# Kernel optimization log

Hardware: AMD Instinct MI355X
Metric: run time of the kernel (lower is better)

Reference implementation:

```python
import jax, jax.numpy as jnp
import numpy as np

DIM, HEADS, WIN = 256, 8, 8
HD = DIM // HEADS
SCALE = HD ** -0.5


def _rel_index(w):
    # Swin-style relative position index, computed statically in numpy
    coords = np.stack(np.meshgrid(np.arange(w), np.arange(w), indexing='ij'))  # (2,w,w)
    cf = coords.reshape(2, -1)                      # (2, w*w)
    rel = (cf[:, :, None] - cf[:, None, :]).transpose(1, 2, 0)  # (w*w, w*w, 2)
    rel = rel.copy()
    rel[:, :, 0] += w - 1
    rel[:, :, 1] += w - 1
    rel[:, :, 0] *= 2 * w - 1
    return rel.sum(-1)                              # (w*w, w*w)

REL_IDX = _rel_index(WIN)


def setup_inputs() -> dict:
    key = jax.random.key(0)
    ks = jax.random.split(key, 6)
    B, C, D, H, W = 8, DIM, 100, WIN, WIN
    return {
        'x': jax.random.normal(ks[0], (B, C, D, H, W), jnp.float32),
        'dwconv_w': jax.random.normal(ks[1], (C, C, 1, 3, 3), jnp.float32) * 0.02,
        'dwconv_b': jnp.zeros((C,), jnp.float32),
        'qkv_w': jax.random.normal(ks[2], (3 * C, C), jnp.float32) * 0.02,
        'qkv_b': jnp.zeros((3 * C,), jnp.float32),
        'proj_w': jax.random.normal(ks[3], (C, C), jnp.float32) * 0.02,
        'proj_b': jnp.zeros((C,), jnp.float32),
        'rpb_table': jax.random.normal(ks[4], ((2 * WIN - 1) ** 2, HEADS), jnp.float32) * 0.02,
    }


def reference(x, dwconv_w, dwconv_b, qkv_w, qkv_b, proj_w, proj_b, rpb_table):
    B, C, D, H, W = x.shape
    N = H * W
    # 'dwconv': full Conv3d, kernel (1,3,3), padding (0,1,1)
    xl = jax.lax.conv_general_dilated(
        x, dwconv_w, window_strides=(1, 1, 1),
        padding=[(0, 0), (1, 1), (1, 1)],
        dimension_numbers=('NCDHW', 'OIDHW', 'NCDHW'),
    ) + dwconv_b[None, :, None, None, None]
    # qkv: 1x1x1 conv == pointwise linear over channels
    qkv = jnp.einsum('oc,bcdhw->bodhw', qkv_w, xl) + qkv_b[None, :, None, None, None]
    # channel dim layout: (three, head, head_dim)
    qkv = qkv.reshape(B, 3, HEADS, HD, D, N)
    q, k, v = qkv[:, 0], qkv[:, 1], qkv[:, 2]      # each (B, HEADS, HD, D, N)
    attn = jnp.einsum('bhcdn,bhcdm->bdhnm', q * SCALE, k)  # (B, D, HEADS, N, N)
    bias = rpb_table[REL_IDX.reshape(-1)].reshape(N, N, HEADS).transpose(2, 0, 1)
    attn = jax.nn.softmax(attn + bias[None, None], axis=-1)
    xa = jnp.einsum('bdhnm,bhcdm->bhcdn', attn, v)  # (B, HEADS, HD, D, N)
    xa = xa.reshape(B, C, D, H, W)                  # channel = (head, head_dim)
    out = jnp.einsum('oc,bcdhw->bodhw', proj_w, xa) + proj_b[None, :, None, None, None]
    return out
```

## Files before the change

kernel.cpp:

```cpp
#include <hip/hip_runtime.h>
#include <cstdint>
#include <cstddef>

#define SCALEQ 0.17677669529663689f

typedef _Float16 half_t;
typedef _Float16 half8   __attribute__((ext_vector_type(8)));
typedef _Float16 half4v  __attribute__((ext_vector_type(4)));
typedef float    float4v __attribute__((ext_vector_type(4)));

#define GLDS16(gp, lp)                                                        \
  __builtin_amdgcn_global_load_lds(                                           \
      (const __attribute__((address_space(1))) void*)(gp),                    \
      (__attribute__((address_space(3))) void*)(lp), 16, 0, 0)

#define WAIT_LDS()                                                            \
  do {                                                                        \
    asm volatile("s_waitcnt lgkmcnt(0)" ::: "memory");                        \
    __builtin_amdgcn_sched_barrier(0);                                        \
  } while (0)

__global__ __launch_bounds__(256) void prep_all(
    const float* __restrict__ x, const float* __restrict__ dwconv_w,
    const float* __restrict__ qkv_w, const float* __restrict__ proj_w,
    const float* __restrict__ rpb, half_t* __restrict__ xq,
    half_t* __restrict__ Wt, half_t* __restrict__ qw16,
    half_t* __restrict__ pw16, float* __restrict__ btab) {
  __shared__ float tile[128 * 65];
  const int blk = blockIdx.x, t = threadIdx.x;
  if (blk < 800) {
    const int bd = blk, b = bd / 100, d = bd % 100;
    for (int hf = 0; hf < 2; ++hf) {
      for (int i = 0; i < 32; ++i) {
        int idx = i * 256 + t, c = idx >> 6, hw = idx & 63;
        tile[c * 65 + hw] = x[(size_t)((b * 256 + hf * 128 + c) * 100 + d) * 64 + hw];
      }
      __syncthreads();
#pragma unroll
      for (int i = 0; i < 4; ++i) {
        int chunk = i * 256 + t;
        int hw = chunk >> 4, c8 = chunk & 15;
        half8 h;
#pragma unroll
        for (int j = 0; j < 8; ++j) h[j] = (half_t)tile[(c8 * 8 + j) * 65 + hw];
        *(half8*)(xq + (size_t)(bd * 64 + hw) * 256 + hf * 128 + c8 * 8) = h;
      }
      __syncthreads();
    }
  } else if (blk < 944) {
    const int base = (blk - 800) * 4096;
#pragma unroll
    for (int i = 0; i < 16; ++i) {
      int idx = base + i * 256 + t;
      int tap = idx >> 16;
      int og = (idx >> 12) & 15, kh = (idx >> 9) & 7;
      int l15o = (idx >> 5) & 15, c5 = idx & 31;
      int o = og * 16 + l15o, c = kh * 32 + c5;
      Wt[idx] = (half_t)dwconv_w[(o * 256 + c) * 9 + tap];
    }
  } else if (blk < 1040) {
    const int base = (blk - 944) * 2048;
#pragma unroll
    for (int i = 0; i < 8; ++i) {
      int idx = base + i * 256 + t;
      float v = qkv_w[idx];
      if (idx < 65536) v *= SCALEQ;
      qw16[idx] = (half_t)v;
    }
  } else if (blk < 1072) {
    const int base = (blk - 1040) * 2048;
#pragma unroll
    for (int i = 0; i < 8; ++i) {
      int idx = base + i * 256 + t;
      pw16[idx] = (half_t)proj_w[idx];
    }
  } else {
    const int base = (blk - 1072) * 2048;
#pragma unroll
    for (int i = 0; i < 8; ++i) {
      int idx = base + i * 256 + t;
      int hd = idx >> 12, n = (idx >> 6) & 63, m = idx & 63;
      int h1 = n >> 3, w1 = n & 7, h2 = m >> 3, w2 = m & 7;
      int ridx = (h1 - h2 + 7) * 15 + (w1 - w2 + 7);
      btab[idx] = rpb[ridx * 8 + hd];
    }
  }
}

__global__ __launch_bounds__(512)
__attribute__((amdgpu_waves_per_eu(4, 4))) void fused_all(
    const half_t* __restrict__ xqg, const half_t* __restrict__ Wt,
    const float* __restrict__ convb, const half_t* __restrict__ qw,
    const float* __restrict__ qkvb, const float* __restrict__ btab,
    const half_t* __restrict__ pw, const float* __restrict__ projb,
    float* __restrict__ out32) {
  __shared__ __align__(16) half_t LS[36864];
  const int bd = blockIdx.x;
  const int tid = threadIdx.x;
  const int wave = tid >> 6, lane = tid & 63;
  const int l15 = lane & 15, quad = lane >> 4;
  const int head = wave;

  half_t* xlp = LS;
  half_t* xa = LS;
  float* T = (float*)LS;
  half_t* xpl = LS + 16384;
  half_t* buf = LS + 16384 + wave * 2560;

  const half_t* Wq0 = qw + head * 32 * 256;
  const half_t* Wk0 = qw + 65536 + head * 32 * 256;
  const half_t* Wv0 = qw + 131072 + head * 32 * 256;

  {
    const char* src = (const char*)(xqg + (size_t)bd * 16384);
    const int cid = wave * 64 + lane;
#pragma unroll
    for (int i = 0; i < 4; ++i) {
      const int chunkid = i * 512 + cid;
      const int row = chunkid >> 5, p = chunkid & 31;
      const int g = (p & 24) | ((p ^ row) & 7);
      GLDS16(src + row * 512 + g * 16, (char*)xpl + (i * 512 + wave * 64) * 16);
    }
    if (tid < 32) {
      half8 z = {};
      *(half8*)(xpl + 64 * 256 + tid * 8) = z;
    }
  }
  __syncthreads();

  {
    const int wwl = l15 & 7, hb = l15 >> 3;
    float4v acc[2][4];
#pragma unroll
    for (int mi = 0; mi < 2; ++mi)
#pragma unroll
      for (int ni = 0; ni < 4; ++ni) {
        float4v z = {0.f, 0.f, 0.f, 0.f};
        acc[mi][ni] = z;
      }
    const half_t* wv0 = Wt + (wave * 2) * 4096 + l15 * 32 + quad * 8;
#pragma unroll 1
    for (int tap = 0; tap < 9; ++tap) {
      const int th = tap / 3, tw = tap - th * 3;
      const half_t* wt = wv0 + tap * 65536;
      const int ww = wwl + tw;
      const int okw = (ww >= 1) & (ww <= 8);
      int rowv[4];
#pragma unroll
      for (int ni = 0; ni < 4; ++ni) {
        const int hh = hb + th + ni * 2;
        const int ok = okw & (hh >= 1) & (hh <= 8);
        rowv[ni] = ok ? ((hh - 1) * 8 + (ww - 1)) : 64;
      }
#pragma unroll
      for (int kh = 0; kh < 8; ++kh) {
        half8 af0 = *(const half8*)(wt + kh * 512);
        half8 af1 = *(const half8*)(wt + 4096 + kh * 512);
        half8 bf[4];
#pragma unroll
        for (int ni = 0; ni < 4; ++ni) {
          const int r = rowv[ni];
          bf[ni] = *(const half8*)&xpl[r * 256 + (((kh * 4 + quad) ^ (r & 7)) * 8)];
        }
#pragma unroll
        for (int ni = 0; ni < 4; ++ni) {
          acc[0][ni] = __builtin_amdgcn_mfma_f32_16x16x32_f16(af0, bf[ni], acc[0][ni], 0, 0, 0);
          acc[1][ni] = __builtin_amdgcn_mfma_f32_16x16x32_f16(af1, bf[ni], acc[1][ni], 0, 0, 0);
        }
      }
    }
#pragma unroll
    for (int mi = 0; mi < 2; ++mi) {
      const int o4 = wave * 32 + mi * 16 + quad * 4;
      const float4v b4 = *(const float4v*)&convb[o4];
      const int chunk = o4 >> 3;
      const int sub = (quad & 1) * 4;
#pragma unroll
      for (int ni = 0; ni < 4; ++ni) {
        const int px = ni * 16 + l15;
        half4v h;
        h.x = (half_t)(acc[mi][ni].x + b4.x);
        h.y = (half_t)(acc[mi][ni].y + b4.y);
        h.z = (half_t)(acc[mi][ni].z + b4.z);
        h.w = (half_t)(acc[mi][ni].w + b4.w);
        *(half4v*)&xlp[px * 256 + ((chunk ^ (px & 7)) * 8) + sub] = h;
      }
    }
  }

  __syncthreads();

  half8 aq[4];
  {
    float4v acc[2][4];
#pragma unroll
    for (int mi = 0; mi < 2; ++mi)
#pragma unroll
      for (int ni = 0; ni < 4; ++ni) {
        float4v z = {0.f, 0.f, 0.f, 0.f};
        acc[mi][ni] = z;
      }
#pragma unroll
    for (int kh = 0; kh < 8; ++kh) {
      half8 w0 = *(const half8*)(Wq0 + l15 * 256 + kh * 32 + quad * 8);
      half8 w1 = *(const half8*)(Wq0 + (16 + l15) * 256 + kh * 32 + quad * 8);
      half8 bf[4];
#pragma unroll
      for (int ni = 0; ni < 4; ++ni) {
        int r = ni * 16 + l15;
        bf[ni] = *(const half8*)&xlp[r * 256 + (((kh * 4 + quad) ^ (r & 7)) * 8)];
      }
#pragma unroll
      for (int ni = 0; ni < 4; ++ni) {
        acc[0][ni] = __builtin_amdgcn_mfma_f32_16x16x32_f16(w0, bf[ni], acc[0][ni], 0, 0, 0);
        acc[1][ni] = __builtin_amdgcn_mfma_f32_16x16x32_f16(w1, bf[ni], acc[1][ni], 0, 0, 0);
      }
    }
#pragma unroll
    for (int mi = 0; mi < 2; ++mi) {
      const float4v b4 = *(const float4v*)&qkvb[head * 32 + mi * 16 + quad * 4];
#pragma unroll
      for (int ni = 0; ni < 4; ++ni) {
        half4v h;
        h.x = (half_t)(acc[mi][ni].x + b4.x * SCALEQ);
        h.y = (half_t)(acc[mi][ni].y + b4.y * SCALEQ);
        h.z = (half_t)(acc[mi][ni].z + b4.z * SCALEQ);
        h.w = (half_t)(acc[mi][ni].w + b4.w * SCALEQ);
        *(half4v*)(buf + (ni * 16 + l15) * 40 + mi * 16 + quad * 4) = h;
      }
    }
    WAIT_LDS();
#pragma unroll
    for (int i = 0; i < 4; ++i)
      aq[i] = *(const half8*)(buf + (i * 16 + l15) * 40 + quad * 8);
    WAIT_LDS();
  }

  half8 bk[4];
  {
    float4v acc[2][4];
#pragma unroll
    for (int mi = 0; mi < 2; ++mi)
#pragma unroll
      for (int ni = 0; ni < 4; ++ni) {
        float4v z = {0.f, 0.f, 0.f, 0.f};
        acc[mi][ni] = z;
      }
#pragma unroll
    for (int kh = 0; kh < 8; ++kh) {
      half8 w0 = *(const half8*)(Wk0 + l15 * 256 + kh * 32 + quad * 8);
      half8 w1 = *(const half8*)(Wk0 + (16 + l15) * 256 + kh * 32 + quad * 8);
      half8 bf[4];
#pragma unroll
      for (int ni = 0; ni < 4; ++ni) {
        int r = ni * 16 + l15;
        bf[ni] = *(const half8*)&xlp[r * 256 + (((kh * 4 + quad) ^ (r & 7)) * 8)];
      }
#pragma unroll
      for (int ni = 0; ni < 4; ++ni) {
        acc[0][ni] = __builtin_amdgcn_mfma_f32_16x16x32_f16(w0, bf[ni], acc[0][ni], 0, 0, 0);
        acc[1][ni] = __builtin_amdgcn_mfma_f32_16x16x32_f16(w1, bf[ni], acc[1][ni], 0, 0, 0);
      }
    }
#pragma unroll
    for (int mi = 0; mi < 2; ++mi) {
      const float4v b4 = *(const float4v*)&qkvb[256 + head * 32 + mi * 16 + quad * 4];
#pragma unroll
      for (int ni = 0; ni < 4; ++ni) {
        half4v h;
        h.x = (half_t)(acc[mi][ni].x + b4.x);
        h.y = (half_t)(acc[mi][ni].y + b4.y);
        h.z = (half_t)(acc[mi][ni].z + b4.z);
        h.w = (half_t)(acc[mi][ni].w + b4.w);
        *(half4v*)(buf + (ni * 16 + l15) * 40 + mi * 16 + quad * 4) = h;
      }
    }
    WAIT_LDS();
#pragma unroll
    for (int i = 0; i < 4; ++i)
      bk[i] = *(const half8*)(buf + (i * 16 + l15) * 40 + quad * 8);
    WAIT_LDS();
  }

  {
    float4v acc[2][4];
#pragma unroll
    for (int mi = 0; mi < 2; ++mi)
#pragma unroll
      for (int ni = 0; ni < 4; ++ni) {
        float4v z = {0.f, 0.f, 0.f, 0.f};
        acc[mi][ni] = z;
      }
#pragma unroll
    for (int kh = 0; kh < 8; ++kh) {
      half8 w0 = *(const half8*)(Wv0 + l15 * 256 + kh * 32 + quad * 8);
      half8 w1 = *(const half8*)(Wv0 + (16 + l15) * 256 + kh * 32 + quad * 8);
      half8 bf[4];
#pragma unroll
      for (int ni = 0; ni < 4; ++ni) {
        int r = ni * 16 + l15;
        bf[ni] = *(const half8*)&xlp[r * 256 + (((kh * 4 + quad) ^ (r & 7)) * 8)];
      }
#pragma unroll
      for (int ni = 0; ni < 4; ++ni) {
        acc[0][ni] = __builtin_amdgcn_mfma_f32_16x16x32_f16(w0, bf[ni], acc[0][ni], 0, 0, 0);
        acc[1][ni] = __builtin_amdgcn_mfma_f32_16x16x32_f16(w1, bf[ni], acc[1][ni], 0, 0, 0);
      }
    }
#pragma unroll
    for (int mi = 0; mi < 2; ++mi) {
      const float4v b4 = *(const float4v*)&qkvb[512 + head * 32 + mi * 16 + quad * 4];
#pragma unroll
      for (int ni = 0; ni < 4; ++ni) {
#pragma unroll
        for (int iv = 0; iv < 4; ++iv)
          buf[(mi * 16 + quad * 4 + iv) * 72 + ni * 16 + l15] =
              (half_t)(acc[mi][ni][iv] + b4[iv]);
      }
    }
  }

  const float* bh = btab + head * 4096;
  float4v s[4][4];
#pragma unroll
  for (int ni = 0; ni < 4; ++ni)
#pragma unroll
    for (int mi = 0; mi < 4; ++mi) {
      float4v z = {0.f, 0.f, 0.f, 0.f};
      s[ni][mi] = __builtin_amdgcn_mfma_f32_16x16x32_f16(aq[ni], bk[mi], z, 0, 0, 0);
    }
#pragma unroll
  for (int ni = 0; ni < 4; ++ni)
#pragma unroll
    for (int i = 0; i < 4; ++i) {
      const int n = ni * 16 + quad * 4 + i;
#pragma unroll
      for (int mi = 0; mi < 4; ++mi)
        s[ni][mi][i] += bh[n * 64 + mi * 16 + l15];
    }
  float inv[4][4];
#pragma unroll
  for (int ni = 0; ni < 4; ++ni)
#pragma unroll
    for (int i = 0; i < 4; ++i) {
      float mx = fmaxf(fmaxf(s[ni][0][i], s[ni][1][i]), fmaxf(s[ni][2][i], s[ni][3][i]));
      for (int off = 1; off < 16; off <<= 1) mx = fmaxf(mx, __shfl_xor(mx, off));
      float sum = 0.f;
#pragma unroll
      for (int mi = 0; mi < 4; ++mi) {
        float e = __expf(s[ni][mi][i] - mx);
        s[ni][mi][i] = e;
        sum += e;
      }
      for (int off = 1; off < 16; off <<= 1) sum += __shfl_xor(sum, off);
      inv[ni][i] = 1.0f / sum;
    }
  half4v ph[4][4];
#pragma unroll
  for (int ni = 0; ni < 4; ++ni)
#pragma unroll
    for (int mi = 0; mi < 4; ++mi)
#pragma unroll
      for (int i = 0; i < 4; ++i)
        ph[ni][mi][i] = (half_t)(s[ni][mi][i] * inv[ni][i]);

  WAIT_LDS();
  half8 av[2][2];
#pragma unroll
  for (int ci = 0; ci < 2; ++ci)
#pragma unroll
    for (int k2 = 0; k2 < 2; ++k2)
      av[ci][k2] = *(const half8*)(buf + (ci * 16 + l15) * 72 + k2 * 32 + quad * 8);
  WAIT_LDS();

  float4v oa[2][4];
#pragma unroll
  for (int ci = 0; ci < 2; ++ci)
#pragma unroll
    for (int ni = 0; ni < 4; ++ni) {
      float4v z = {0.f, 0.f, 0.f, 0.f};
      oa[ci][ni] = z;
    }
#pragma unroll
  for (int k2 = 0; k2 < 2; ++k2) {
#pragma unroll
    for (int mi2 = 0; mi2 < 2; ++mi2) {
      const int mi = k2 * 2 + mi2;
#pragma unroll
      for (int ni = 0; ni < 4; ++ni)
#pragma unroll
        for (int i = 0; i < 4; ++i) {
          const int n = ni * 16 + quad * 4 + i;
          buf[n * 40 + mi2 * 16 + l15] = ph[ni][mi][i];
        }
    }
    WAIT_LDS();
    half8 bp[4];
#pragma unroll
    for (int ni = 0; ni < 4; ++ni)
      bp[ni] = *(const half8*)(buf + (ni * 16 + l15) * 40 + quad * 8);
    WAIT_LDS();
#pragma unroll
    for (int ni = 0; ni < 4; ++ni)
#pragma unroll
      for (int ci = 0; ci < 2; ++ci)
        oa[ci][ni] = __builtin_amdgcn_mfma_f32_16x16x32_f16(av[ci][k2], bp[ni], oa[ci][ni], 0, 0, 0);
  }

  __syncthreads();

#pragma unroll
  for (int ci = 0; ci < 2; ++ci)
#pragma unroll
    for (int ni = 0; ni < 4; ++ni) {
      half4v h = {(half_t)oa[ci][ni].x, (half_t)oa[ci][ni].y,
                  (half_t)oa[ci][ni].z, (half_t)oa[ci][ni].w};
      *(half4v*)(xa + (ni * 16 + l15) * 264 + head * 32 + ci * 16 + quad * 4) = h;
    }
  __syncthreads();

  const half_t* Wp0 = pw + wave * 32 * 256;
  float4v pacc[2][4];
#pragma unroll
  for (int mi = 0; mi < 2; ++mi)
#pragma unroll
    for (int ni = 0; ni < 4; ++ni) {
      float4v z = {0.f, 0.f, 0.f, 0.f};
      pacc[mi][ni] = z;
    }
#pragma unroll
  for (int kh = 0; kh < 8; ++kh) {
    half8 w0 = *(const half8*)(Wp0 + l15 * 256 + kh * 32 + quad * 8);
    half8 w1 = *(const half8*)(Wp0 + (16 + l15) * 256 + kh * 32 + quad * 8);
    half8 bf[4];
#pragma unroll
    for (int ni = 0; ni < 4; ++ni)
      bf[ni] = *(const half8*)&xa[(ni * 16 + l15) * 264 + kh * 32 + quad * 8];
#pragma unroll
    for (int ni = 0; ni < 4; ++ni) {
      pacc[0][ni] = __builtin_amdgcn_mfma_f32_16x16x32_f16(w0, bf[ni], pacc[0][ni], 0, 0, 0);
      pacc[1][ni] = __builtin_amdgcn_mfma_f32_16x16x32_f16(w1, bf[ni], pacc[1][ni], 0, 0, 0);
    }
  }
#pragma unroll
  for (int mi = 0; mi < 2; ++mi) {
    const float4v b4 = *(const float4v*)&projb[wave * 32 + mi * 16 + quad * 4];
#pragma unroll
    for (int ni = 0; ni < 4; ++ni) {
      pacc[mi][ni].x += b4.x;
      pacc[mi][ni].y += b4.y;
      pacc[mi][ni].z += b4.z;
      pacc[mi][ni].w += b4.w;
    }
  }

  const int b = bd / 100, d = bd % 100;
  const size_t bdbase = (size_t)b * 1638400 + (size_t)d * 64;
  const int tr = tid >> 3;
  const int col0 = (tid & 7) * 4;
  for (int r = 0; r < 4; ++r) {
    __syncthreads();
    if ((wave >> 1) == r) {
      const int rb = (wave & 1) * 32;
#pragma unroll
      for (int mi = 0; mi < 2; ++mi)
#pragma unroll
        for (int ni = 0; ni < 4; ++ni)
#pragma unroll
          for (int iv = 0; iv < 4; ++iv)
            T[(rb + mi * 16 + quad * 4 + iv) * 68 + ni * 16 + l15] = pacc[mi][ni][iv];
    }
    __syncthreads();
    const int o = r * 64 + tr;
    float* dst = out32 + bdbase + (size_t)o * 6400 + col0;
    const float* srcT = &T[tr * 68 + col0];
    float4v v0 = *(const float4v*)srcT;
    float4v v1 = *(const float4v*)(srcT + 32);
    __builtin_nontemporal_store(v0, (float4v*)dst);
    __builtin_nontemporal_store(v1, (float4v*)(dst + 32));
  }
}

extern "C" void kernel_launch(void* const* d_in, const int* in_sizes, int n_in,
                              void* d_out, int out_size, void* d_ws, size_t ws_size,
                              hipStream_t stream) {
  const float* x        = (const float*)d_in[0];
  const float* dwconv_w = (const float*)d_in[1];
  const float* dwconv_b = (const float*)d_in[2];
  const float* qkv_w    = (const float*)d_in[3];
  const float* qkv_b    = (const float*)d_in[4];
  const float* proj_w   = (const float*)d_in[5];
  const float* proj_b   = (const float*)d_in[6];
  const float* rpb      = (const float*)d_in[7];
  float* out = (float*)d_out;

  char* ws = (char*)d_ws;
  size_t off = 0;
  half_t* xq   = (half_t*)(ws + off); off += 26214400;
  half_t* Wt   = (half_t*)(ws + off); off += 1179648;
  half_t* qw16 = (half_t*)(ws + off); off += 393216;
  half_t* pw16 = (half_t*)(ws + off); off += 131072;
  float*  btab = (float*)(ws + off);  off += 131072;

  prep_all<<<1088, 256, 0, stream>>>(x, dwconv_w, qkv_w, proj_w, rpb,
                                     xq, Wt, qw16, pw16, btab);
  fused_all<<<800, 512, 0, stream>>>(xq, Wt, dwconv_b, qw16, qkv_b, btab,
                                     pw16, proj_b, out);
}
```

Before: 269.7 us.

## Shrink LDS footprint to raise occupancy by reading conv input from global

The conv stage now reads its input tile straight from global memory, with a padded zero row added to the prep-stage layout, instead of staging it in LDS. The per-wave LDS scratch is halved by transposing Q, K, V and P in two halves, and occupancy is raised from 4 to 6 waves per EU. This trades LDS traffic and its bank-swizzled reads for uncached-in-LDS global/L2 reads during the conv, and the larger wave count may push up register pressure.

```diff
diff --git a/kernel.cpp b/kernel.cpp
--- a/kernel.cpp
+++ b/kernel.cpp
@@ -8,11 +8,6 @@
 typedef _Float16 half8   __attribute__((ext_vector_type(8)));
 typedef _Float16 half4v  __attribute__((ext_vector_type(4)));
 typedef float    float4v __attribute__((ext_vector_type(4)));
-
-#define GLDS16(gp, lp)                                                        \
-  __builtin_amdgcn_global_load_lds(                                           \
-      (const __attribute__((address_space(1))) void*)(gp),                    \
-      (__attribute__((address_space(3))) void*)(lp), 16, 0, 0)
 
 #define WAIT_LDS()                                                            \
   do {                                                                        \
@@ -30,6 +25,10 @@
   const int blk = blockIdx.x, t = threadIdx.x;
   if (blk < 800) {
     const int bd = blk, b = bd / 100, d = bd % 100;
+    if (t < 32) {
+      half8 z = {};
+      *(half8*)(xq + ((size_t)bd * 65 + 64) * 256 + t * 8) = z;
+    }
     for (int hf = 0; hf < 2; ++hf) {
       for (int i = 0; i < 32; ++i) {
         int idx = i * 256 + t, c = idx >> 6, hw = idx & 63;
@@ -43,7 +42,7 @@
         half8 h;
 #pragma unroll
         for (int j = 0; j < 8; ++j) h[j] = (half_t)tile[(c8 * 8 + j) * 65 + hw];
-        *(half8*)(xq + (size_t)(bd * 64 + hw) * 256 + hf * 128 + c8 * 8) = h;
+        *(half8*)(xq + ((size_t)bd * 65 + hw) * 256 + hf * 128 + c8 * 8) = h;
       }
       __syncthreads();
     }
@@ -88,13 +87,13 @@
 }
 
 __global__ __launch_bounds__(512)
-__attribute__((amdgpu_waves_per_eu(4, 4))) void fused_all(
+__attribute__((amdgpu_waves_per_eu(6, 6))) void fused_all(
     const half_t* __restrict__ xqg, const half_t* __restrict__ Wt,
     const float* __restrict__ convb, const half_t* __restrict__ qw,
     const float* __restrict__ qkvb, const float* __restrict__ btab,
     const half_t* __restrict__ pw, const float* __restrict__ projb,
     float* __restrict__ out32) {
-  __shared__ __align__(16) half_t LS[36864];
+  __shared__ __align__(16) half_t LS[26624];
   const int bd = blockIdx.x;
   const int tid = threadIdx.x;
   const int wave = tid >> 6, lane = tid & 63;
@@ -104,29 +103,12 @@
   half_t* xlp = LS;
   half_t* xa = LS;
   float* T = (float*)LS;
-  half_t* xpl = LS + 16384;
-  half_t* buf = LS + 16384 + wave * 2560;
+  half_t* buf = LS + 16384 + wave * 1280;
 
   const half_t* Wq0 = qw + head * 32 * 256;
   const half_t* Wk0 = qw + 65536 + head * 32 * 256;
   const half_t* Wv0 = qw + 131072 + head * 32 * 256;
-
-  {
-    const char* src = (const char*)(xqg + (size_t)bd * 16384);
-    const int cid = wave * 64 + lane;
-#pragma unroll
-    for (int i = 0; i < 4; ++i) {
-      const int chunkid = i * 512 + cid;
-      const int row = chunkid >> 5, p = chunkid & 31;
-      const int g = (p & 24) | ((p ^ row) & 7);
-      GLDS16(src + row * 512 + g * 16, (char*)xpl + (i * 512 + wave * 64) * 16);
-    }
-    if (tid < 32) {
-      half8 z = {};
-      *(half8*)(xpl + 64 * 256 + tid * 8) = z;
-    }
-  }
-  __syncthreads();
+  const half_t* xb = xqg + (size_t)bd * 16640;
 
   {
     const int wwl = l15 & 7, hb = l15 >> 3;
@@ -158,10 +140,8 @@
         half8 af1 = *(const half8*)(wt + 4096 + kh * 512);
         half8 bf[4];
 #pragma unroll
-        for (int ni = 0; ni < 4; ++ni) {
-          const int r = rowv[ni];
-          bf[ni] = *(const half8*)&xpl[r * 256 + (((kh * 4 + quad) ^ (r & 7)) * 8)];
-        }
+        for (int ni = 0; ni < 4; ++ni)
+          bf[ni] = *(const half8*)(xb + rowv[ni] * 256 + kh * 32 + quad * 8);
 #pragma unroll
         for (int ni = 0; ni < 4; ++ni) {
           acc[0][ni] = __builtin_amdgcn_mfma_f32_16x16x32_f16(af0, bf[ni], acc[0][ni], 0, 0, 0);
@@ -217,23 +197,27 @@
       }
     }
 #pragma unroll
-    for (int mi = 0; mi < 2; ++mi) {
-      const float4v b4 = *(const float4v*)&qkvb[head * 32 + mi * 16 + quad * 4];
-#pragma unroll
-      for (int ni = 0; ni < 4; ++ni) {
-        half4v h;
-        h.x = (half_t)(acc[mi][ni].x + b4.x * SCALEQ);
-        h.y = (half_t)(acc[mi][ni].y + b4.y * SCALEQ);
-        h.z = (half_t)(acc[mi][ni].z + b4.z * SCALEQ);
-        h.w = (half_t)(acc[mi][ni].w + b4.w * SCALEQ);
-        *(half4v*)(buf + (ni * 16 + l15) * 40 + mi * 16 + quad * 4) = h;
-      }
-    }
-    WAIT_LDS();
-#pragma unroll
-    for (int i = 0; i < 4; ++i)
-      aq[i] = *(const half8*)(buf + (i * 16 + l15) * 40 + quad * 8);
-    WAIT_LDS();
+    for (int h2 = 0; h2 < 2; ++h2) {
+#pragma unroll
+      for (int mi = 0; mi < 2; ++mi) {
+        const float4v b4 = *(const float4v*)&qkvb[head * 32 + mi * 16 + quad * 4];
+#pragma unroll
+        for (int nj = 0; nj < 2; ++nj) {
+          const int ni = h2 * 2 + nj;
+          half4v h;
+          h.x = (half_t)(acc[mi][ni].x + b4.x * SCALEQ);
+          h.y = (half_t)(acc[mi][ni].y + b4.y * SCALEQ);
+          h.z = (half_t)(acc[mi][ni].z + b4.z * SCALEQ);
+          h.w = (half_t)(acc[mi][ni].w + b4.w * SCALEQ);
+          *(half4v*)(buf + (nj * 16 + l15) * 40 + mi * 16 + quad * 4) = h;
+        }
+      }
+      WAIT_LDS();
+#pragma unroll
+      for (int j = 0; j < 2; ++j)
+        aq[h2 * 2 + j] = *(const half8*)(buf + (j * 16 + l15) * 40 + quad * 8);
+      WAIT_LDS();
+    }
   }
 
   half8 bk[4];
@@ -263,25 +247,30 @@
       }
     }
 #pragma unroll
-    for (int mi = 0; mi < 2; ++mi) {
-      const float4v b4 = *(const float4v*)&qkvb[256 + head * 32 + mi * 16 + quad * 4];
-#pragma unroll
-      for (int ni = 0; ni < 4; ++ni) {
-        half4v h;
-        h.x = (half_t)(acc[mi][ni].x + b4.x);
-        h.y = (half_t)(acc[mi][ni].y + b4.y);
-        h.z = (half_t)(acc[mi][ni].z + b4.z);
-        h.w = (half_t)(acc[mi][ni].w + b4.w);
-        *(half4v*)(buf + (ni * 16 + l15) * 40 + mi * 16 + quad * 4) = h;
-      }
-    }
-    WAIT_LDS();
-#pragma unroll
-    for (int i = 0; i < 4; ++i)
-      bk[i] = *(const half8*)(buf + (i * 16 + l15) * 40 + quad * 8);
-    WAIT_LDS();
-  }
-
+    for (int h2 = 0; h2 < 2; ++h2) {
+#pragma unroll
+      for (int mi = 0; mi < 2; ++mi) {
+        const float4v b4 = *(const float4v*)&qkvb[256 + head * 32 + mi * 16 + quad * 4];
+#pragma unroll
+        for (int nj = 0; nj < 2; ++nj) {
+          const int ni = h2 * 2 + nj;
+          half4v h;
+          h.x = (half_t)(acc[mi][ni].x + b4.x);
+          h.y = (half_t)(acc[mi][ni].y + b4.y);
+          h.z = (half_t)(acc[mi][ni].z + b4.z);
+          h.w = (half_t)(acc[mi][ni].w + b4.w);
+          *(half4v*)(buf + (nj * 16 + l15) * 40 + mi * 16 + quad * 4) = h;
+        }
+      }
+      WAIT_LDS();
+#pragma unroll
+      for (int j = 0; j < 2; ++j)
+        bk[h2 * 2 + j] = *(const half8*)(buf + (j * 16 + l15) * 40 + quad * 8);
+      WAIT_LDS();
+    }
+  }
+
+  half8 av[2][2];
   {
     float4v acc[2][4];
 #pragma unroll
@@ -311,12 +300,16 @@
     for (int mi = 0; mi < 2; ++mi) {
       const float4v b4 = *(const float4v*)&qkvb[512 + head * 32 + mi * 16 + quad * 4];
 #pragma unroll
-      for (int ni = 0; ni < 4; ++ni) {
+      for (int ni = 0; ni < 4; ++ni)
 #pragma unroll
         for (int iv = 0; iv < 4; ++iv)
-          buf[(mi * 16 + quad * 4 + iv) * 72 + ni * 16 + l15] =
+          buf[(quad * 4 + iv) * 72 + ni * 16 + l15] =
               (half_t)(acc[mi][ni][iv] + b4[iv]);
-      }
+      WAIT_LDS();
+#pragma unroll
+      for (int k2 = 0; k2 < 2; ++k2)
+        av[mi][k2] = *(const half8*)(buf + l15 * 72 + k2 * 32 + quad * 8);
+      WAIT_LDS();
     }
   }
 
@@ -364,15 +357,6 @@
       for (int i = 0; i < 4; ++i)
         ph[ni][mi][i] = (half_t)(s[ni][mi][i] * inv[ni][i]);
 
-  WAIT_LDS();
-  half8 av[2][2];
-#pragma unroll
-  for (int ci = 0; ci < 2; ++ci)
-#pragma unroll
-    for (int k2 = 0; k2 < 2; ++k2)
-      av[ci][k2] = *(const half8*)(buf + (ci * 16 + l15) * 72 + k2 * 32 + quad * 8);
-  WAIT_LDS();
-
   float4v oa[2][4];
 #pragma unroll
   for (int ci = 0; ci < 2; ++ci)
@@ -384,27 +368,31 @@
 #pragma unroll
   for (int k2 = 0; k2 < 2; ++k2) {
 #pragma unroll
-    for (int mi2 = 0; mi2 < 2; ++mi2) {
-      const int mi = k2 * 2 + mi2;
-#pragma unroll
-      for (int ni = 0; ni < 4; ++ni)
-#pragma unroll
-        for (int i = 0; i < 4; ++i) {
-          const int n = ni * 16 + quad * 4 + i;
-          buf[n * 40 + mi2 * 16 + l15] = ph[ni][mi][i];
+    for (int rh = 0; rh < 2; ++rh) {
+#pragma unroll
+      for (int nj = 0; nj < 2; ++nj) {
+        const int ni = rh * 2 + nj;
+#pragma unroll
+        for (int mi2 = 0; mi2 < 2; ++mi2) {
+          const int mi = k2 * 2 + mi2;
+#pragma unroll
+          for (int i = 0; i < 4; ++i)
+            buf[(nj * 16 + quad * 4 + i) * 36 + mi2 * 16 + l15] = ph[ni][mi][i];
         }
-    }
-    WAIT_LDS();
-    half8 bp[4];
-#pragma unroll
-    for (int ni = 0; ni < 4; ++ni)
-      bp[ni] = *(const half8*)(buf + (ni * 16 + l15) * 40 + quad * 8);
-    WAIT_LDS();
-#pragma unroll
-    for (int ni = 0; ni < 4; ++ni)
-#pragma unroll
-      for (int ci = 0; ci < 2; ++ci)
-        oa[ci][ni] = __builtin_amdgcn_mfma_f32_16x16x32_f16(av[ci][k2], bp[ni], oa[ci][ni], 0, 0, 0);
+      }
+      WAIT_LDS();
+      half8 bpn[2];
+#pragma unroll
+      for (int nj = 0; nj < 2; ++nj)
+        bpn[nj] = *(const half8*)(buf + (nj * 16 + l15) * 36 + quad * 8);
+      WAIT_LDS();
+#pragma unroll
+      for (int nj = 0; nj < 2; ++nj)
+#pragma unroll
+        for (int ci = 0; ci < 2; ++ci)
+          oa[ci][rh * 2 + nj] = __builtin_amdgcn_mfma_f32_16x16x32_f16(
+              av[ci][k2], bpn[nj], oa[ci][rh * 2 + nj], 0, 0, 0);
+    }
   }
 
   __syncthreads();
@@ -496,7 +484,7 @@
 
   char* ws = (char*)d_ws;
   size_t off = 0;
-  half_t* xq   = (half_t*)(ws + off); off += 26214400;
+  half_t* xq   = (half_t*)(ws + off); off += 26624000;
   half_t* Wt   = (half_t*)(ws + off); off += 1179648;
   half_t* qw16 = (half_t*)(ws + off); off += 393216;
   half_t* pw16 = (half_t*)(ws + off); off += 131072;
```

Result: slower. 561.5 us (+108.2%).

## Fuse input transpose and fp16 cast into main fused kernel

Applied to the files above, without the earlier changes.

Removes the per-(b,d) transpose/convert stage from the prep kernel and has the fused kernel read fp32 x directly, transpose it through LDS, convert it to half and write the swizzled layout. This drops a 26 MB intermediate write and its read-back, and shrinks the prep grid. In exchange the main kernel does extra LDS round trips, two more barriers and strided global reads before the conv stage can start.

```diff
diff --git a/kernel.cpp b/kernel.cpp
--- a/kernel.cpp
+++ b/kernel.cpp
@@ -8,11 +8,6 @@
 typedef _Float16 half8   __attribute__((ext_vector_type(8)));
 typedef _Float16 half4v  __attribute__((ext_vector_type(4)));
 typedef float    float4v __attribute__((ext_vector_type(4)));
-
-#define GLDS16(gp, lp)                                                        \
-  __builtin_amdgcn_global_load_lds(                                           \
-      (const __attribute__((address_space(1))) void*)(gp),                    \
-      (__attribute__((address_space(3))) void*)(lp), 16, 0, 0)
 
 #define WAIT_LDS()                                                            \
   do {                                                                        \
@@ -20,35 +15,14 @@
     __builtin_amdgcn_sched_barrier(0);                                        \
   } while (0)
 
-__global__ __launch_bounds__(256) void prep_all(
-    const float* __restrict__ x, const float* __restrict__ dwconv_w,
-    const float* __restrict__ qkv_w, const float* __restrict__ proj_w,
-    const float* __restrict__ rpb, half_t* __restrict__ xq,
+__global__ __launch_bounds__(256) void prep_w(
+    const float* __restrict__ dwconv_w, const float* __restrict__ qkv_w,
+    const float* __restrict__ proj_w, const float* __restrict__ rpb,
     half_t* __restrict__ Wt, half_t* __restrict__ qw16,
     half_t* __restrict__ pw16, float* __restrict__ btab) {
-  __shared__ float tile[128 * 65];
   const int blk = blockIdx.x, t = threadIdx.x;
-  if (blk < 800) {
-    const int bd = blk, b = bd / 100, d = bd % 100;
-    for (int hf = 0; hf < 2; ++hf) {
-      for (int i = 0; i < 32; ++i) {
-        int idx = i * 256 + t, c = idx >> 6, hw = idx & 63;
-        tile[c * 65 + hw] = x[(size_t)((b * 256 + hf * 128 + c) * 100 + d) * 64 + hw];
-      }
-      __syncthreads();
-#pragma unroll
-      for (int i = 0; i < 4; ++i) {
-        int chunk = i * 256 + t;
-        int hw = chunk >> 4, c8 = chunk & 15;
-        half8 h;
-#pragma unroll
-        for (int j = 0; j < 8; ++j) h[j] = (half_t)tile[(c8 * 8 + j) * 65 + hw];
-        *(half8*)(xq + (size_t)(bd * 64 + hw) * 256 + hf * 128 + c8 * 8) = h;
-      }
-      __syncthreads();
-    }
-  } else if (blk < 944) {
-    const int base = (blk - 800) * 4096;
+  if (blk < 144) {
+    const int base = blk * 4096;
 #pragma unroll
     for (int i = 0; i < 16; ++i) {
       int idx = base + i * 256 + t;
@@ -58,8 +32,8 @@
       int o = og * 16 + l15o, c = kh * 32 + c5;
       Wt[idx] = (half_t)dwconv_w[(o * 256 + c) * 9 + tap];
     }
-  } else if (blk < 1040) {
-    const int base = (blk - 944) * 2048;
+  } else if (blk < 240) {
+    const int base = (blk - 144) * 2048;
 #pragma unroll
     for (int i = 0; i < 8; ++i) {
       int idx = base + i * 256 + t;
@@ -67,15 +41,15 @@
       if (idx < 65536) v *= SCALEQ;
       qw16[idx] = (half_t)v;
     }
-  } else if (blk < 1072) {
-    const int base = (blk - 1040) * 2048;
+  } else if (blk < 272) {
+    const int base = (blk - 240) * 2048;
 #pragma unroll
     for (int i = 0; i < 8; ++i) {
       int idx = base + i * 256 + t;
       pw16[idx] = (half_t)proj_w[idx];
     }
   } else {
-    const int base = (blk - 1072) * 2048;
+    const int base = (blk - 272) * 2048;
 #pragma unroll
     for (int i = 0; i < 8; ++i) {
       int idx = base + i * 256 + t;
@@ -89,7 +63,7 @@
 
 __global__ __launch_bounds__(512)
 __attribute__((amdgpu_waves_per_eu(4, 4))) void fused_all(
-    const half_t* __restrict__ xqg, const half_t* __restrict__ Wt,
+    const float* __restrict__ xg, const half_t* __restrict__ Wt,
     const float* __restrict__ convb, const half_t* __restrict__ qw,
     const float* __restrict__ qkvb, const float* __restrict__ btab,
     const half_t* __restrict__ pw, const float* __restrict__ projb,
@@ -100,26 +74,44 @@
   const int wave = tid >> 6, lane = tid & 63;
   const int l15 = lane & 15, quad = lane >> 4;
   const int head = wave;
+  const int b = bd / 100, d = bd % 100;
 
   half_t* xlp = LS;
   half_t* xa = LS;
   float* T = (float*)LS;
   half_t* xpl = LS + 16384;
   half_t* buf = LS + 16384 + wave * 2560;
+  float* tile = (float*)LS;
 
   const half_t* Wq0 = qw + head * 32 * 256;
   const half_t* Wk0 = qw + 65536 + head * 32 * 256;
   const half_t* Wv0 = qw + 131072 + head * 32 * 256;
 
   {
-    const char* src = (const char*)(xqg + (size_t)bd * 16384);
-    const int cid = wave * 64 + lane;
+    const float* xb0 = xg + ((size_t)(b * 256) * 100 + d) * 64;
+#pragma unroll
+    for (int i = 0; i < 32; ++i) {
+      const int c = i * 8 + wave;
+      tile[c * 66 + lane] = xb0[(size_t)c * 6400 + lane];
+    }
+  }
+  __syncthreads();
+
+  half8 xr[4];
+#pragma unroll
+  for (int i = 0; i < 4; ++i) {
+    const int c8 = wave * 4 + i;
+#pragma unroll
+    for (int j = 0; j < 8; ++j)
+      xr[i][j] = (half_t)tile[(c8 * 8 + j) * 66 + lane];
+  }
+  __syncthreads();
+
+  {
 #pragma unroll
     for (int i = 0; i < 4; ++i) {
-      const int chunkid = i * 512 + cid;
-      const int row = chunkid >> 5, p = chunkid & 31;
-      const int g = (p & 24) | ((p ^ row) & 7);
-      GLDS16(src + row * 512 + g * 16, (char*)xpl + (i * 512 + wave * 64) * 16);
+      const int c8 = wave * 4 + i;
+      *(half8*)&xpl[lane * 256 + ((c8 ^ (lane & 7)) * 8)] = xr[i];
     }
     if (tid < 32) {
       half8 z = {};
@@ -454,7 +446,6 @@
     }
   }
 
-  const int b = bd / 100, d = bd % 100;
   const size_t bdbase = (size_t)b * 1638400 + (size_t)d * 64;
   const int tr = tid >> 3;
   const int col0 = (tid & 7) * 4;
@@ -496,14 +487,13 @@
 
   char* ws = (char*)d_ws;
   size_t off = 0;
-  half_t* xq   = (half_t*)(ws + off); off += 26214400;
   half_t* Wt   = (half_t*)(ws + off); off += 1179648;
   half_t* qw16 = (half_t*)(ws + off); off += 393216;
   half_t* pw16 = (half_t*)(ws + off); off += 131072;
   float*  btab = (float*)(ws + off);  off += 131072;
 
-  prep_all<<<1088, 256, 0, stream>>>(x, dwconv_w, qkv_w, proj_w, rpb,
-                                     xq, Wt, qw16, pw16, btab);
-  fused_all<<<800, 512, 0, stream>>>(xq, Wt, dwconv_b, qw16, qkv_b, btab,
+  prep_w<<<288, 256, 0, stream>>>(dwconv_w, qkv_w, proj_w, rpb,
+                                  Wt, qw16, pw16, btab);
+  fused_all<<<800, 512, 0, stream>>>(x, Wt, dwconv_b, qw16, qkv_b, btab,
                                      pw16, proj_b, out);
 }
```

After: 265.6 us. No clear change (-1.5%).
